# Optimization experiments

Hardware: AMD Instinct MI355X
Metric: run time of the kernel (lower is better)

Reference implementation:

```python
import jax, jax.numpy as jnp
import numpy as np
from jax import lax

NX = 4096
NY = 4096
NLEVEL = 13  # int(log2(min(nx, ny))) + 1
OMEGA = 1.0
DN = ('NCHW', 'OIHW', 'NCHW')


def _bc(u):
    # torch boundary_condition: replicate edges into a zero-padded frame; corners stay 0
    up = jnp.pad(u, ((0, 0), (0, 0), (1, 1), (1, 1)), mode='edge')
    up = up.at[0, 0, 0, 0].set(0.0)
    up = up.at[0, 0, 0, -1].set(0.0)
    up = up.at[0, 0, -1, 0].set(0.0)
    up = up.at[0, 0, -1, -1].set(0.0)
    return up


def _prol(x):
    return jnp.repeat(jnp.repeat(x, 2, axis=2), 2, axis=3)


def setup_inputs() -> dict:
    key = jax.random.key(0)
    k1, k2 = jax.random.split(key)
    # realistic 5-point-like stencil with strong diagonal + randn perturbation
    base = jnp.array([[0.0, 1.0, 0.0], [1.0, 4.0, 1.0], [0.0, 1.0, 0.0]], dtype=jnp.float32)
    A = base + 0.01 * jax.random.normal(k1, (3, 3), dtype=jnp.float32)
    u0 = jax.random.normal(k2, (1, 1, NY, NX), dtype=jnp.float32)
    return {"A": A, "u0": u0, "t": 4}


def reference(A, u0, t):
    diag = A[1, 1]                      # center extracted before zeroing, as in __init__
    K = (A.at[1, 1].set(0.0))[None, None]  # (1,1,3,3) smoothing kernel, zero center
    KR = jnp.full((1, 1, 2, 2), 0.25, dtype=A.dtype)  # restriction kernel

    def smooth(x):
        return lax.conv_general_dilated(x, K, (1, 1), 'VALID', dimension_numbers=DN)

    def restrict(x):
        return lax.conv_general_dilated(x, KR, (2, 2), 'VALID', dimension_numbers=DN)

    b = 0.0
    u = u0
    for _ in range(t):
        r = smooth(_bc(u)) - b  # (1,1,NY,NX)
        r_s = [r]
        for _i in range(1, NLEVEL - 5):
            r = restrict(r)
            r_s.append(r)
        e = jnp.zeros((1, 1, 1, 1), dtype=A.dtype)
        for j in reversed(range(1, NLEVEL - 5)):
            e_pad = jnp.pad(e, ((0, 0), (0, 0), (1, 1), (1, 1)))
            e = e - smooth(e_pad) / diag + r_s[j] / diag  # broadcasts to r_s[j] shape
            e = _prol(e)
        u_update = u - e - smooth(_bc(u)) / diag + b / diag
        u = (1.0 - OMEGA) * u + OMEGA * u_update
    return (u - u.min()) / (u.max() - u.min())
```

## Files before the change

kernel.cpp:

```cpp
#include <hip/hip_runtime.h>

#define N 4096

__device__ __forceinline__ float bf2f(unsigned short h)
{
    unsigned int u = ((unsigned int)h) << 16;
    return __uint_as_float(u);
}
__device__ __forceinline__ unsigned short f2bf(float f)
{
    unsigned int x = __float_as_uint(f);
    unsigned int r = (x + 0x7FFFu + ((x >> 16) & 1u)) >> 16;
    return (unsigned short)r;
}

__device__ __forceinline__ void load_A(const float* __restrict__ Ag,
                                       float Ac[3][3], float& inv)
{
#pragma unroll
    for (int i = 0; i < 9; ++i) Ac[i / 3][i % 3] = Ag[i];
    inv = 1.0f / Ac[1][1];
    Ac[1][1] = 0.f;
}

__device__ __forceinline__ void make_w44(const float Ac[3][3], float wt[4][4])
{
#pragma unroll
    for (int a = 0; a < 4; ++a)
#pragma unroll
        for (int b = 0; b < 4; ++b) wt[a][b] = 0.f;
#pragma unroll
    for (int r = 0; r < 2; ++r)
#pragma unroll
        for (int c = 0; c < 2; ++c)
#pragma unroll
            for (int i = 0; i < 3; ++i)
#pragma unroll
                for (int j = 0; j < 3; ++j) wt[r + i][c + j] += Ac[i][j];
}

template <typename TI>
__device__ __forceinline__ void load_row6T(const TI* __restrict__ u,
                                           int gy, int xm, int colL, int colR,
                                           bool cornL, bool cornR, bool yedge,
                                           float v[6])
{
    int cy = min(max(gy, 0), N - 1);
    const TI* rowp = &u[(size_t)cy * N];
    float L, R;
    if constexpr (sizeof(TI) == 4) {
        float4 m = *(const float4*)&rowp[xm];
        v[1] = m.x; v[2] = m.y; v[3] = m.z; v[4] = m.w;
        L = rowp[colL];
        R = rowp[colR];
    } else {
        ushort4 m = *(const ushort4*)&rowp[xm];
        v[1] = bf2f(m.x); v[2] = bf2f(m.y); v[3] = bf2f(m.z); v[4] = bf2f(m.w);
        L = bf2f(rowp[colL]);
        R = bf2f(rowp[colR]);
    }
    if (yedge) {
        bool oob = (gy < 0) | (gy >= N);
        if (oob & cornL) L = 0.f;
        if (oob & cornR) R = 0.f;
    }
    v[0] = L; v[5] = R;
}

__device__ __forceinline__ void swz2048(int bid, int& bx, int& by)
{
    int reg = (bid & 7) * 256 + (bid >> 3);
    bx = reg & 15;
    by = reg >> 4;
}

template <typename TI>
__global__ __launch_bounds__(256) void smooth_restrict2_kernel(
    const TI* __restrict__ u, const float* __restrict__ Ag,
    unsigned short* __restrict__ r2, float* __restrict__ r3)
{
    int t = threadIdx.x, lane = t & 63, w = t >> 6;
    int bx, by;
    swz2048(blockIdx.x, bx, by);
    int x0 = 256 * bx;
    int Y0 = 16 * by + 4 * w;
    int gy0 = 2 * Y0 - 1;
    bool yedge = (gy0 < 0) | (gy0 + 9 >= N);
    float Ac[3][3], inv;
    load_A(Ag, Ac, inv);
    float wt[4][4];
    make_w44(Ac, wt);

    int xm = x0 + 4 * lane;
    int colL = max(xm - 1, 0), colR = min(xm + 4, N - 1);
    bool cornL = (xm - 1 < 0), cornR = (xm + 4 >= N);
    float v[10][6];
#pragma unroll
    for (int rr = 0; rr < 10; ++rr)
        load_row6T<TI>(u, gy0 + rr, xm, colL, colR, cornL, cornR, yedge, v[rr]);

    float o0[4], o1[4];
#pragma unroll
    for (int q = 0; q < 4; ++q) {
        float a0 = 0.f, a1 = 0.f;
#pragma unroll
        for (int a = 0; a < 4; ++a) {
            const float* vv = v[2 * q + a];
#pragma unroll
            for (int b = 0; b < 4; ++b) {
                a0 += wt[a][b] * vv[b];
                a1 += wt[a][b] * vv[b + 2];
            }
        }
        o0[q] = 0.25f * a0;
        o1[q] = 0.25f * a1;
    }
    int Y2 = Y0 >> 1, X2 = 64 * bx + lane;
    float val0 = 0.25f * (o0[0] + o1[0] + o0[1] + o1[1]);
    float val1 = 0.25f * (o0[2] + o1[2] + o0[3] + o1[3]);
    r2[(size_t)Y2 * 1024 + X2] = f2bf(val0);
    r2[(size_t)(Y2 + 1) * 1024 + X2] = f2bf(val1);
    float s0 = val0 + val1;
    float s1 = __shfl_xor(s0, 1);
    if (!(lane & 1))
        r3[(size_t)(Y2 >> 1) * 512 + (X2 >> 1)] = 0.25f * (s0 + s1);
}

__global__ __launch_bounds__(256) void multirestrict_kernel(
    const float* __restrict__ r3, float* __restrict__ r4, float* __restrict__ r5,
    float* __restrict__ r6, float* __restrict__ r7)
{
    int BX = blockIdx.x, BY = blockIdx.y;
    __shared__ float s4[16][17];
    __shared__ float s5[8][9];
    __shared__ float s6[4][5];
    int t = threadIdx.x;
    {
        int y = t >> 4, x = t & 15;
        const float* b0 = &r3[(size_t)(32 * BY + 2 * y) * 512 + 32 * BX + 2 * x];
        float2 a = *(const float2*)b0;
        float2 b = *(const float2*)(b0 + 512);
        float vv = 0.25f * (a.x + a.y + b.x + b.y);
        r4[(size_t)(16 * BY + y) * 256 + 16 * BX + x] = vv;
        s4[y][x] = vv;
    }
    __syncthreads();
    if (t < 64) {
        int y = t >> 3, x = t & 7;
        float vv = 0.25f * (s4[2 * y][2 * x] + s4[2 * y][2 * x + 1] +
                            s4[2 * y + 1][2 * x] + s4[2 * y + 1][2 * x + 1]);
        r5[(size_t)(8 * BY + y) * 128 + 8 * BX + x] = vv;
        s5[y][x] = vv;
    }
    __syncthreads();
    if (t < 16) {
        int y = t >> 2, x = t & 3;
        float vv = 0.25f * (s5[2 * y][2 * x] + s5[2 * y][2 * x + 1] +
                            s5[2 * y + 1][2 * x] + s5[2 * y + 1][2 * x + 1]);
        r6[(size_t)(4 * BY + y) * 64 + 4 * BX + x] = vv;
        s6[y][x] = vv;
    }
    __syncthreads();
    if (t < 4) {
        int y = t >> 1, x = t & 1;
        float vv = 0.25f * (s6[2 * y][2 * x] + s6[2 * y][2 * x + 1] +
                            s6[2 * y + 1][2 * x] + s6[2 * y + 1][2 * x + 1]);
        r7[(size_t)(2 * BY + y) * 32 + 2 * BX + x] = vv;
    }
}

__global__ __launch_bounds__(256) void coarse_up_kernel(
    const float* __restrict__ r7, const float* __restrict__ r6,
    const float* __restrict__ r5, const float* __restrict__ r4,
    const float* __restrict__ r3, const float* __restrict__ Ag,
    float* __restrict__ e512)
{
    int bx = blockIdx.x, by = blockIdx.y;
    int t = threadIdx.x;
    __shared__ float s7[32][33];
    __shared__ float s64[64][65];
    __shared__ float s128[11][12];
    __shared__ float s256[18][19];
    float Ac[3][3], inv;
    load_A(Ag, Ac, inv);
    for (int i = t; i < 1024; i += 256) s7[i >> 5][i & 31] = r7[i] * inv;
    __syncthreads();
    for (int i = t; i < 4096; i += 256) {
        int y = i >> 6, x = i & 63;
        float ctr = s7[y >> 1][x >> 1];
        float sm = 0.f;
#pragma unroll
        for (int dy = -1; dy <= 1; ++dy)
#pragma unroll
            for (int dx = -1; dx <= 1; ++dx) {
                if (dy == 0 && dx == 0) continue;
                int yy = y + dy, xx = x + dx;
                float pe = 0.f;
                if (yy >= 0 && yy < 64 && xx >= 0 && xx < 64) pe = s7[yy >> 1][xx >> 1];
                sm += Ac[dy + 1][dx + 1] * pe;
            }
        s64[y][x] = ctr - sm * inv + r6[i] * inv;
    }
    __syncthreads();
    int R1 = 8 * by - 2, C1 = 8 * bx - 2;
    if (t < 121) {
        int pr = t / 11, pc = t % 11;
        int gy = R1 + pr, gx = C1 + pc;
        if (gy >= 0 && gy < 128 && gx >= 0 && gx < 128) {
            float ctr = s64[gy >> 1][gx >> 1];
            float sm = 0.f;
#pragma unroll
            for (int dy = -1; dy <= 1; ++dy)
#pragma unroll
                for (int dx = -1; dx <= 1; ++dx) {
                    if (dy == 0 && dx == 0) continue;
                    int yy = gy + dy, xx = gx + dx;
                    float pe = 0.f;
                    if (yy >= 0 && yy < 128 && xx >= 0 && xx < 128) pe = s64[yy >> 1][xx >> 1];
                    sm += Ac[dy + 1][dx + 1] * pe;
                }
            s128[pr][pc] = ctr - sm * inv + r5[(size_t)gy * 128 + gx] * inv;
        }
    }
    __syncthreads();
    int R2l = 16 * by - 1, C2l = 16 * bx - 1;
    for (int i = t; i < 324; i += 256) {
        int pr = i / 18, pc = i % 18;
        int gy = R2l + pr, gx = C2l + pc;
        if (gy >= 0 && gy < 256 && gx >= 0 && gx < 256) {
            float ctr = s128[(gy >> 1) - R1][(gx >> 1) - C1];
            float sm = 0.f;
#pragma unroll
            for (int dy = -1; dy <= 1; ++dy)
#pragma unroll
                for (int dx = -1; dx <= 1; ++dx) {
                    if (dy == 0 && dx == 0) continue;
                    int yy = gy + dy, xx = gx + dx;
                    float pe = 0.f;
                    if (yy >= 0 && yy < 256 && xx >= 0 && xx < 256)
                        pe = s128[(yy >> 1) - R1][(xx >> 1) - C1];
                    sm += Ac[dy + 1][dx + 1] * pe;
                }
            s256[pr][pc] = ctr - sm * inv + r4[(size_t)gy * 256 + gx] * inv;
        }
    }
    __syncthreads();
#pragma unroll
    for (int k = 0; k < 4; ++k) {
        int idx = t + 256 * k;
        int y = 32 * by + (idx >> 5), x = 32 * bx + (idx & 31);
        float ctr = s256[(y >> 1) - R2l][(x >> 1) - C2l];
        float sm = 0.f;
#pragma unroll
        for (int dy = -1; dy <= 1; ++dy)
#pragma unroll
            for (int dx = -1; dx <= 1; ++dx) {
                if (dy == 0 && dx == 0) continue;
                int yy = y + dy, xx = x + dx;
                float pe = 0.f;
                if (yy >= 0 && yy < 512 && xx >= 0 && xx < 512)
                    pe = s256[(yy >> 1) - R2l][(xx >> 1) - C2l];
                sm += Ac[dy + 1][dx + 1] * pe;
            }
        e512[(size_t)y * 512 + x] = ctr - sm * inv + r3[(size_t)y * 512 + x] * inv;
    }
}

template <typename TI, typename TO, bool WANTMM>
__global__ __launch_bounds__(256) void final_fused_kernel(
    const TI* __restrict__ u, const float* __restrict__ e512,
    const unsigned short* __restrict__ r2, const float* __restrict__ Ag,
    TO* __restrict__ uo, float* __restrict__ partials)
{
    const int n = N;
    int t = threadIdx.x, lane = t & 63, w = t >> 6;
    int bx, by;
    swz2048(blockIdx.x, bx, by);
    int x0 = 256 * bx, y0 = 32 * by;
    __shared__ float s512v[6][36];
    __shared__ float s1024[10][68];
    float Ac[3][3], inv;
    load_A(Ag, Ac, inv);
    float wt[4][4];
    make_w44(Ac, wt);

    int yb = y0 + 8 * w;
    int gy0 = yb - 1;
    bool yedge = (gy0 < 0) | (gy0 + 9 >= n);
    int xm = x0 + 4 * lane;
    int colL = max(xm - 1, 0), colR = min(xm + 4, n - 1);
    bool cornL = (xm - 1 < 0), cornR = (xm + 4 >= n);
    float v[10][6];
#pragma unroll
    for (int rr = 0; rr < 10; ++rr)
        load_row6T<TI>(u, gy0 + rr, xm, colL, colR, cornL, cornR, yedge, v[rr]);

    int S5r = 4 * by - 1, S5c = 32 * bx - 1;
    if (t < 216) {
        int pr = t / 36, pc = t - (t / 36) * 36;
        int gy = S5r + pr, gx = S5c + pc;
        float vv = 0.f;
        if (pc < 34 && gy >= 0 && gy < 512 && gx >= 0 && gx < 512)
            vv = e512[(size_t)gy * 512 + gx];
        s512v[pr][pc] = vv;
    }
    __syncthreads();
    int R10 = 8 * by - 1, C10 = 64 * bx - 1;
    for (int i = t; i < 680; i += 256) {
        int pr = i / 68, pc = i - (i / 68) * 68;
        if (pc < 66) {
            int gy = R10 + pr, gx = C10 + pc;
            float val = 0.f;
            if (gy >= 0 && gy < 1024 && gx >= 0 && gx < 1024) {
                float ctr = s512v[(gy >> 1) - S5r][(gx >> 1) - S5c];
                float sm = 0.f;
#pragma unroll
                for (int dy = -1; dy <= 1; ++dy)
#pragma unroll
                    for (int dx = -1; dx <= 1; ++dx) {
                        if (dy == 0 && dx == 0) continue;
                        sm += Ac[dy + 1][dx + 1] *
                              s512v[((gy + dy) >> 1) - S5r][((gx + dx) >> 1) - S5c];
                    }
                val = ctr - sm * inv + bf2f(r2[(size_t)gy * 1024 + gx]) * inv;
            }
            s1024[pr][pc] = val;
        }
    }
    __syncthreads();
    float e2[4][2];
    int EY0 = 16 * by + 4 * w, EX0 = 128 * bx + 2 * lane;
#pragma unroll
    for (int a = 0; a < 4; ++a) {
        int gy = EY0 + a;
        float a0 = 0.f, a1 = 0.f;
#pragma unroll
        for (int i = 0; i < 4; ++i) {
            const float* vv = v[2 * a + i];
#pragma unroll
            for (int j = 0; j < 4; ++j) {
                a0 += wt[i][j] * vv[j];
                a1 += wt[i][j] * vv[j + 2];
            }
        }
        float r1v[2] = {0.25f * a0, 0.25f * a1};
#pragma unroll
        for (int b = 0; b < 2; ++b) {
            int gx = EX0 + b;
            float ctr = s1024[(gy >> 1) - R10][(gx >> 1) - C10];
            float sm = 0.f;
#pragma unroll
            for (int dy = -1; dy <= 1; ++dy)
#pragma unroll
                for (int dx = -1; dx <= 1; ++dx) {
                    if (dy == 0 && dx == 0) continue;
                    sm += Ac[dy + 1][dx + 1] *
                          s1024[((gy + dy) >> 1) - R10][((gx + dx) >> 1) - C10];
                }
            e2[a][b] = ctr - sm * inv + r1v[b] * inv;
        }
    }
    float mn = 3.402823466e+38f, mx = -3.402823466e+38f;
#pragma unroll
    for (int r = 0; r < 8; ++r) {
        int y = yb + r;
        const float* va = v[r];
        const float* vb = v[r + 1];
        const float* vc = v[r + 2];
        float out[4];
#pragma unroll
        for (int c = 0; c < 4; ++c) {
            float sm = Ac[0][0] * va[c] + Ac[0][1] * va[c + 1] + Ac[0][2] * va[c + 2]
                     + Ac[1][0] * vb[c]                        + Ac[1][2] * vb[c + 2]
                     + Ac[2][0] * vc[c] + Ac[2][1] * vc[c + 1] + Ac[2][2] * vc[c + 2];
            out[c] = vb[c + 1] - e2[r >> 1][c >> 1] - sm * inv;
        }
        if constexpr (sizeof(TO) == 4) {
            *(float4*)&uo[(size_t)y * n + xm] =
                make_float4(out[0], out[1], out[2], out[3]);
        } else {
            ushort4 o;
            o.x = f2bf(out[0]); o.y = f2bf(out[1]);
            o.z = f2bf(out[2]); o.w = f2bf(out[3]);
            *(ushort4*)&uo[(size_t)y * n + xm] = o;
        }
        if (WANTMM) {
            mn = fminf(mn, fminf(fminf(out[0], out[1]), fminf(out[2], out[3])));
            mx = fmaxf(mx, fmaxf(fmaxf(out[0], out[1]), fmaxf(out[2], out[3])));
        }
    }
    if (WANTMM) {
#pragma unroll
        for (int off = 32; off > 0; off >>= 1) {
            mn = fminf(mn, __shfl_down(mn, off));
            mx = fmaxf(mx, __shfl_down(mx, off));
        }
        __shared__ float smn[4], smx[4];
        if (lane == 0) { smn[w] = mn; smx[w] = mx; }
        __syncthreads();
        if (t == 0) {
            mn = smn[0]; mx = smx[0];
            for (int wq = 1; wq < 4; ++wq) { mn = fminf(mn, smn[wq]); mx = fmaxf(mx, smx[wq]); }
            int bid = by * 16 + bx;
            partials[2 * bid] = mn;
            partials[2 * bid + 1] = mx;
        }
    }
}

__global__ __launch_bounds__(1024) void minmax_final_kernel(
    const float* __restrict__ partials, float* __restrict__ mm)
{
    float mn = 3.402823466e+38f, mx = -3.402823466e+38f;
    for (int i = threadIdx.x; i < 2048; i += 1024) {
        mn = fminf(mn, partials[2 * i]);
        mx = fmaxf(mx, partials[2 * i + 1]);
    }
#pragma unroll
    for (int off = 32; off > 0; off >>= 1) {
        mn = fminf(mn, __shfl_down(mn, off));
        mx = fmaxf(mx, __shfl_down(mx, off));
    }
    __shared__ float smn[16], smx[16];
    int lane = threadIdx.x & 63, wv = threadIdx.x >> 6;
    if (lane == 0) { smn[wv] = mn; smx[wv] = mx; }
    __syncthreads();
    if (threadIdx.x == 0) {
        mn = smn[0]; mx = smx[0];
        for (int w = 1; w < 16; ++w) { mn = fminf(mn, smn[w]); mx = fmaxf(mx, smx[w]); }
        mm[0] = mn;
        mm[1] = mx;
    }
}

__global__ __launch_bounds__(256) void normalize_kernel(
    const unsigned short* __restrict__ uin, float* __restrict__ uout,
    const float* __restrict__ mm)
{
    size_t i = ((size_t)blockIdx.x * 256 + threadIdx.x) * 4;
    float mn = mm[0];
    float sc = 1.0f / (mm[1] - mm[0]);
    ushort4 h = *(const ushort4*)&uin[i];
    float4 v;
    v.x = (bf2f(h.x) - mn) * sc;
    v.y = (bf2f(h.y) - mn) * sc;
    v.z = (bf2f(h.z) - mn) * sc;
    v.w = (bf2f(h.w) - mn) * sc;
    *(float4*)&uout[i] = v;
}

extern "C" void kernel_launch(void* const* d_in, const int* in_sizes, int n_in,
                              void* d_out, int out_size, void* d_ws, size_t ws_size,
                              hipStream_t stream)
{
    const float* A  = (const float*)d_in[0];
    const float* u0 = (const float*)d_in[1];
    float* uout = (float*)d_out;
    char* ws = (char*)d_ws;

    size_t off = 0;
    auto alloc_f = [&](size_t nelem) { float* p = (float*)(ws + off); off += nelem * 4; return p; };
    float* r3 = alloc_f(512ull * 512);
    float* r4 = alloc_f(256ull * 256);
    float* r5 = alloc_f(128ull * 128);
    float* r6 = alloc_f(64ull * 64);
    float* r7 = alloc_f(32ull * 32);
    float* e5 = alloc_f(512ull * 512);
    float* partials = alloc_f(4096);
    float* mm = alloc_f(2);
    off = (off + 15) & ~15ull;
    unsigned short* r2 = (unsigned short*)(ws + off); off += 1024ull * 1024 * 2;
    off = (off + 15) & ~15ull;
    unsigned short* ubA = (unsigned short*)(ws + off); off += 4096ull * 4096 * 2;
    unsigned short* ubB = (unsigned short*)(ws + off); off += 4096ull * 4096 * 2;

    for (int it = 0; it < 4; ++it) {
        if (it == 0) {
            smooth_restrict2_kernel<float><<<2048, 256, 0, stream>>>(u0, A, r2, r3);
        } else {
            const unsigned short* us = (it == 2) ? ubB : ubA;
            smooth_restrict2_kernel<unsigned short><<<2048, 256, 0, stream>>>(us, A, r2, r3);
        }
        multirestrict_kernel<<<dim3(16, 16), 256, 0, stream>>>(r3, r4, r5, r6, r7);
        coarse_up_kernel<<<dim3(16, 16), 256, 0, stream>>>(r7, r6, r5, r4, r3, A, e5);
        if (it == 0) {
            final_fused_kernel<float, unsigned short, false><<<2048, 256, 0, stream>>>(
                u0, e5, r2, A, ubA, partials);
        } else if (it == 1) {
            final_fused_kernel<unsigned short, unsigned short, false><<<2048, 256, 0, stream>>>(
                ubA, e5, r2, A, ubB, partials);
        } else if (it == 2) {
            final_fused_kernel<unsigned short, unsigned short, false><<<2048, 256, 0, stream>>>(
                ubB, e5, r2, A, ubA, partials);
        } else {
            final_fused_kernel<unsigned short, unsigned short, true><<<2048, 256, 0, stream>>>(
                ubA, e5, r2, A, ubB, partials);
        }
    }
    minmax_final_kernel<<<1, 1024, 0, stream>>>(partials, mm);
    normalize_kernel<<<16384, 256, 0, stream>>>(ubB, uout, mm);
}
```

Baseline: 205.0 us.

## Fuse coarse-grid correction chain into final kernel with per-block halo recomputation

Removes the separate coarse_up_kernel and the e512 intermediate buffer. Each final_fused_kernel block now rebuilds its own small halo patches of the 64, 128, 256 and 512 level corrections from r7 to r3, using a floor-division helper that handles negative indices. This saves one launch per iteration, plus the global write and read of e512. In exchange, every block does redundant tiny stencil work behind several extra __syncthreads barriers.

```diff
diff --git a/kernel.cpp b/kernel.cpp
--- a/kernel.cpp
+++ b/kernel.cpp
@@ -13,6 +13,8 @@
     unsigned int r = (x + 0x7FFFu + ((x >> 16) & 1u)) >> 16;
     return (unsigned short)r;
 }
+
+__device__ __forceinline__ int cr(int i) { return ((i + 1024) >> 1) - 512; }
 
 __device__ __forceinline__ void load_A(const float* __restrict__ Ag,
                                        float Ac[3][3], float& inv)
@@ -169,114 +171,24 @@
     }
 }
 
-__global__ __launch_bounds__(256) void coarse_up_kernel(
+template <typename TI, typename TO, bool WANTMM>
+__global__ __launch_bounds__(256) void final_fused_kernel(
+    const TI* __restrict__ u,
     const float* __restrict__ r7, const float* __restrict__ r6,
     const float* __restrict__ r5, const float* __restrict__ r4,
-    const float* __restrict__ r3, const float* __restrict__ Ag,
-    float* __restrict__ e512)
-{
-    int bx = blockIdx.x, by = blockIdx.y;
-    int t = threadIdx.x;
-    __shared__ float s7[32][33];
-    __shared__ float s64[64][65];
-    __shared__ float s128[11][12];
-    __shared__ float s256[18][19];
-    float Ac[3][3], inv;
-    load_A(Ag, Ac, inv);
-    for (int i = t; i < 1024; i += 256) s7[i >> 5][i & 31] = r7[i] * inv;
-    __syncthreads();
-    for (int i = t; i < 4096; i += 256) {
-        int y = i >> 6, x = i & 63;
-        float ctr = s7[y >> 1][x >> 1];
-        float sm = 0.f;
-#pragma unroll
-        for (int dy = -1; dy <= 1; ++dy)
-#pragma unroll
-            for (int dx = -1; dx <= 1; ++dx) {
-                if (dy == 0 && dx == 0) continue;
-                int yy = y + dy, xx = x + dx;
-                float pe = 0.f;
-                if (yy >= 0 && yy < 64 && xx >= 0 && xx < 64) pe = s7[yy >> 1][xx >> 1];
-                sm += Ac[dy + 1][dx + 1] * pe;
-            }
-        s64[y][x] = ctr - sm * inv + r6[i] * inv;
-    }
-    __syncthreads();
-    int R1 = 8 * by - 2, C1 = 8 * bx - 2;
-    if (t < 121) {
-        int pr = t / 11, pc = t % 11;
-        int gy = R1 + pr, gx = C1 + pc;
-        if (gy >= 0 && gy < 128 && gx >= 0 && gx < 128) {
-            float ctr = s64[gy >> 1][gx >> 1];
-            float sm = 0.f;
-#pragma unroll
-            for (int dy = -1; dy <= 1; ++dy)
-#pragma unroll
-                for (int dx = -1; dx <= 1; ++dx) {
-                    if (dy == 0 && dx == 0) continue;
-                    int yy = gy + dy, xx = gx + dx;
-                    float pe = 0.f;
-                    if (yy >= 0 && yy < 128 && xx >= 0 && xx < 128) pe = s64[yy >> 1][xx >> 1];
-                    sm += Ac[dy + 1][dx + 1] * pe;
-                }
-            s128[pr][pc] = ctr - sm * inv + r5[(size_t)gy * 128 + gx] * inv;
-        }
-    }
-    __syncthreads();
-    int R2l = 16 * by - 1, C2l = 16 * bx - 1;
-    for (int i = t; i < 324; i += 256) {
-        int pr = i / 18, pc = i % 18;
-        int gy = R2l + pr, gx = C2l + pc;
-        if (gy >= 0 && gy < 256 && gx >= 0 && gx < 256) {
-            float ctr = s128[(gy >> 1) - R1][(gx >> 1) - C1];
-            float sm = 0.f;
-#pragma unroll
-            for (int dy = -1; dy <= 1; ++dy)
-#pragma unroll
-                for (int dx = -1; dx <= 1; ++dx) {
-                    if (dy == 0 && dx == 0) continue;
-                    int yy = gy + dy, xx = gx + dx;
-                    float pe = 0.f;
-                    if (yy >= 0 && yy < 256 && xx >= 0 && xx < 256)
-                        pe = s128[(yy >> 1) - R1][(xx >> 1) - C1];
-                    sm += Ac[dy + 1][dx + 1] * pe;
-                }
-            s256[pr][pc] = ctr - sm * inv + r4[(size_t)gy * 256 + gx] * inv;
-        }
-    }
-    __syncthreads();
-#pragma unroll
-    for (int k = 0; k < 4; ++k) {
-        int idx = t + 256 * k;
-        int y = 32 * by + (idx >> 5), x = 32 * bx + (idx & 31);
-        float ctr = s256[(y >> 1) - R2l][(x >> 1) - C2l];
-        float sm = 0.f;
-#pragma unroll
-        for (int dy = -1; dy <= 1; ++dy)
-#pragma unroll
-            for (int dx = -1; dx <= 1; ++dx) {
-                if (dy == 0 && dx == 0) continue;
-                int yy = y + dy, xx = x + dx;
-                float pe = 0.f;
-                if (yy >= 0 && yy < 512 && xx >= 0 && xx < 512)
-                    pe = s256[(yy >> 1) - R2l][(xx >> 1) - C2l];
-                sm += Ac[dy + 1][dx + 1] * pe;
-            }
-        e512[(size_t)y * 512 + x] = ctr - sm * inv + r3[(size_t)y * 512 + x] * inv;
-    }
-}
-
-template <typename TI, typename TO, bool WANTMM>
-__global__ __launch_bounds__(256) void final_fused_kernel(
-    const TI* __restrict__ u, const float* __restrict__ e512,
-    const unsigned short* __restrict__ r2, const float* __restrict__ Ag,
-    TO* __restrict__ uo, float* __restrict__ partials)
+    const float* __restrict__ r3, const unsigned short* __restrict__ r2,
+    const float* __restrict__ Ag, TO* __restrict__ uo,
+    float* __restrict__ partials)
 {
     const int n = N;
     int t = threadIdx.x, lane = t & 63, w = t >> 6;
     int bx, by;
     swz2048(blockIdx.x, bx, by);
     int x0 = 256 * bx, y0 = 32 * by;
+    __shared__ float s32p[3][4];
+    __shared__ float s64p[3][6];
+    __shared__ float s128p[3][10];
+    __shared__ float s256p[4][18];
     __shared__ float s512v[6][36];
     __shared__ float s1024[10][68];
     float Ac[3][3], inv;
@@ -285,24 +197,102 @@
     make_w44(Ac, wt);
 
     int yb = y0 + 8 * w;
-    int gy0 = yb - 1;
-    bool yedge = (gy0 < 0) | (gy0 + 9 >= n);
+    int gyu = yb - 1;
+    bool yedge = (gyu < 0) | (gyu + 9 >= n);
     int xm = x0 + 4 * lane;
     int colL = max(xm - 1, 0), colR = min(xm + 4, n - 1);
     bool cornL = (xm - 1 < 0), cornR = (xm + 4 >= n);
     float v[10][6];
 #pragma unroll
     for (int rr = 0; rr < 10; ++rr)
-        load_row6T<TI>(u, gy0 + rr, xm, colL, colR, cornL, cornR, yedge, v[rr]);
-
+        load_row6T<TI>(u, gyu + rr, xm, colL, colR, cornL, cornR, yedge, v[rr]);
+
+    int R32 = (by >> 2) - 1, C32 = 2 * bx - 1;
+    if (t < 12) {
+        int pr = t >> 2, pc = t & 3;
+        int gy = R32 + pr, gx = C32 + pc;
+        s32p[pr][pc] = (gy >= 0 && gy < 32 && gx >= 0 && gx < 32)
+                           ? r7[(size_t)gy * 32 + gx] * inv : 0.f;
+    }
+    __syncthreads();
+    int R64 = (by >> 1) - 1, C64 = 4 * bx - 1;
+    if (t < 18) {
+        int pr = t / 6, pc = t - (t / 6) * 6;
+        int gy = R64 + pr, gx = C64 + pc;
+        float val = 0.f;
+        if (gy >= 0 && gy < 64 && gx >= 0 && gx < 64) {
+            float ctr = s32p[cr(gy) - R32][cr(gx) - C32];
+            float sm = 0.f;
+#pragma unroll
+            for (int dy = -1; dy <= 1; ++dy)
+#pragma unroll
+                for (int dx = -1; dx <= 1; ++dx) {
+                    if (dy == 0 && dx == 0) continue;
+                    sm += Ac[dy + 1][dx + 1] * s32p[cr(gy + dy) - R32][cr(gx + dx) - C32];
+                }
+            val = ctr - sm * inv + r6[(size_t)gy * 64 + gx] * inv;
+        }
+        s64p[pr][pc] = val;
+    }
+    __syncthreads();
+    int R128 = by - 1, C128 = 8 * bx - 1;
+    if (t < 30) {
+        int pr = t / 10, pc = t - (t / 10) * 10;
+        int gy = R128 + pr, gx = C128 + pc;
+        float val = 0.f;
+        if (gy >= 0 && gy < 128 && gx >= 0 && gx < 128) {
+            float ctr = s64p[cr(gy) - R64][cr(gx) - C64];
+            float sm = 0.f;
+#pragma unroll
+            for (int dy = -1; dy <= 1; ++dy)
+#pragma unroll
+                for (int dx = -1; dx <= 1; ++dx) {
+                    if (dy == 0 && dx == 0) continue;
+                    sm += Ac[dy + 1][dx + 1] * s64p[cr(gy + dy) - R64][cr(gx + dx) - C64];
+                }
+            val = ctr - sm * inv + r5[(size_t)gy * 128 + gx] * inv;
+        }
+        s128p[pr][pc] = val;
+    }
+    __syncthreads();
+    int R256 = 2 * by - 1, C256 = 16 * bx - 1;
+    if (t < 72) {
+        int pr = t / 18, pc = t - (t / 18) * 18;
+        int gy = R256 + pr, gx = C256 + pc;
+        float val = 0.f;
+        if (gy >= 0 && gy < 256 && gx >= 0 && gx < 256) {
+            float ctr = s128p[cr(gy) - R128][cr(gx) - C128];
+            float sm = 0.f;
+#pragma unroll
+            for (int dy = -1; dy <= 1; ++dy)
+#pragma unroll
+                for (int dx = -1; dx <= 1; ++dx) {
+                    if (dy == 0 && dx == 0) continue;
+                    sm += Ac[dy + 1][dx + 1] * s128p[cr(gy + dy) - R128][cr(gx + dx) - C128];
+                }
+            val = ctr - sm * inv + r4[(size_t)gy * 256 + gx] * inv;
+        }
+        s256p[pr][pc] = val;
+    }
+    __syncthreads();
     int S5r = 4 * by - 1, S5c = 32 * bx - 1;
     if (t < 216) {
         int pr = t / 36, pc = t - (t / 36) * 36;
         int gy = S5r + pr, gx = S5c + pc;
-        float vv = 0.f;
-        if (pc < 34 && gy >= 0 && gy < 512 && gx >= 0 && gx < 512)
-            vv = e512[(size_t)gy * 512 + gx];
-        s512v[pr][pc] = vv;
+        float val = 0.f;
+        if (pc < 34 && gy >= 0 && gy < 512 && gx >= 0 && gx < 512) {
+            float ctr = s256p[cr(gy) - R256][cr(gx) - C256];
+            float sm = 0.f;
+#pragma unroll
+            for (int dy = -1; dy <= 1; ++dy)
+#pragma unroll
+                for (int dx = -1; dx <= 1; ++dx) {
+                    if (dy == 0 && dx == 0) continue;
+                    sm += Ac[dy + 1][dx + 1] * s256p[cr(gy + dy) - R256][cr(gx + dx) - C256];
+                }
+            val = ctr - sm * inv + r3[(size_t)gy * 512 + gx] * inv;
+        }
+        s512v[pr][pc] = val;
     }
     __syncthreads();
     int R10 = 8 * by - 1, C10 = 64 * bx - 1;
@@ -312,7 +302,7 @@
             int gy = R10 + pr, gx = C10 + pc;
             float val = 0.f;
             if (gy >= 0 && gy < 1024 && gx >= 0 && gx < 1024) {
-                float ctr = s512v[(gy >> 1) - S5r][(gx >> 1) - S5c];
+                float ctr = s512v[cr(gy) - S5r][cr(gx) - S5c];
                 float sm = 0.f;
 #pragma unroll
                 for (int dy = -1; dy <= 1; ++dy)
@@ -320,7 +310,7 @@
                     for (int dx = -1; dx <= 1; ++dx) {
                         if (dy == 0 && dx == 0) continue;
                         sm += Ac[dy + 1][dx + 1] *
-                              s512v[((gy + dy) >> 1) - S5r][((gx + dx) >> 1) - S5c];
+                              s512v[cr(gy + dy) - S5r][cr(gx + dx) - S5c];
                     }
                 val = ctr - sm * inv + bf2f(r2[(size_t)gy * 1024 + gx]) * inv;
             }
@@ -465,7 +455,6 @@
     float* r5 = alloc_f(128ull * 128);
     float* r6 = alloc_f(64ull * 64);
     float* r7 = alloc_f(32ull * 32);
-    float* e5 = alloc_f(512ull * 512);
     float* partials = alloc_f(4096);
     float* mm = alloc_f(2);
     off = (off + 15) & ~15ull;
@@ -482,19 +471,18 @@
             smooth_restrict2_kernel<unsigned short><<<2048, 256, 0, stream>>>(us, A, r2, r3);
         }
         multirestrict_kernel<<<dim3(16, 16), 256, 0, stream>>>(r3, r4, r5, r6, r7);
-        coarse_up_kernel<<<dim3(16, 16), 256, 0, stream>>>(r7, r6, r5, r4, r3, A, e5);
         if (it == 0) {
             final_fused_kernel<float, unsigned short, false><<<2048, 256, 0, stream>>>(
-                u0, e5, r2, A, ubA, partials);
+                u0, r7, r6, r5, r4, r3, r2, A, ubA, partials);
         } else if (it == 1) {
             final_fused_kernel<unsigned short, unsigned short, false><<<2048, 256, 0, stream>>>(
-                ubA, e5, r2, A, ubB, partials);
+                ubA, r7, r6, r5, r4, r3, r2, A, ubB, partials);
         } else if (it == 2) {
             final_fused_kernel<unsigned short, unsigned short, false><<<2048, 256, 0, stream>>>(
-                ubB, e5, r2, A, ubA, partials);
+                ubB, r7, r6, r5, r4, r3, r2, A, ubA, partials);
         } else {
             final_fused_kernel<unsigned short, unsigned short, true><<<2048, 256, 0, stream>>>(
-                ubA, e5, r2, A, ubB, partials);
+                ubA, r7, r6, r5, r4, r3, r2, A, ubB, partials);
         }
     }
     minmax_final_kernel<<<1, 1024, 0, stream>>>(partials, mm);
```

Result: faster. 175.4 us (-14.4%).
